# Optimization experiments

Hardware: AMD Instinct MI355X
Metric: run time of the kernel (lower is better)

The kernel has to match this reference:

```python
import jax, jax.numpy as jnp
import numpy as np

B, S_RAW, S_SUM, D_IN, H, NH = 32, 1024, 128, 300, 256, 4
DH = (2 * H) // NH  # per-head dim = 128


def _lstm_dir(x, Wih, Whh, b, reverse):
    """Single-direction LSTM (PyTorch gate order i,f,g,o). x: [B,S,D] -> [B,S,H]."""
    xg = jnp.einsum('bsd,gd->bsg', x, Wih) + b          # precompute input gates [B,S,4H]
    xg = jnp.swapaxes(xg, 0, 1)                          # [S,B,4H]
    Hh = Whh.shape[1]
    bsz = x.shape[0]

    def step(carry, g):
        h, c = carry
        gates = g + h @ Whh.T
        i, f, gg, o = jnp.split(gates, 4, axis=-1)
        c = jax.nn.sigmoid(f) * c + jax.nn.sigmoid(i) * jnp.tanh(gg)
        h = jax.nn.sigmoid(o) * jnp.tanh(c)
        return (h, c), h

    init = (jnp.zeros((bsz, Hh), x.dtype), jnp.zeros((bsz, Hh), x.dtype))
    _, hs = jax.lax.scan(step, init, xg, reverse=reverse)  # hs aligned with input time order
    return jnp.swapaxes(hs, 0, 1)


def _bilstm(x, pf, pb):
    return jnp.concatenate([_lstm_dir(x, *pf, False), _lstm_dir(x, *pb, True)], axis=-1)


def setup_inputs() -> dict:
    key = jax.random.key(0)
    ks = jax.random.split(key, 24)
    s_lstm = 1.0 / np.sqrt(H)
    s_proj = 1.0 / np.sqrt(2 * H)
    d = {}
    d['in_raw'] = jax.random.normal(ks[0], (B, S_RAW, D_IN), jnp.float32)
    d['in_sum'] = jax.random.normal(ks[1], (B, S_SUM, D_IN), jnp.float32)
    d['len_raw'] = jax.random.randint(ks[2], (B,), 0, S_RAW)
    d['len_sum'] = jax.random.randint(ks[3], (B,), 0, S_SUM)
    i = 4
    for name in ['raw_f', 'raw_b', 'sum_f', 'sum_b']:
        d[name + '_Wih'] = jax.random.uniform(ks[i], (4 * H, D_IN), jnp.float32, -s_lstm, s_lstm); i += 1
        d[name + '_Whh'] = jax.random.uniform(ks[i], (4 * H, H), jnp.float32, -s_lstm, s_lstm); i += 1
        d[name + '_b'] = jax.random.uniform(ks[i], (4 * H,), jnp.float32, -s_lstm, s_lstm); i += 1
    d['Wq'] = jax.random.uniform(ks[i], (NH, 2 * H, DH), jnp.float32, -s_proj, s_proj); i += 1
    d['Wk'] = jax.random.uniform(ks[i], (NH, 2 * H, DH), jnp.float32, -s_proj, s_proj); i += 1
    d['Wv'] = jax.random.uniform(ks[i], (NH, 2 * H, DH), jnp.float32, -s_proj, s_proj)
    return d


def reference(in_raw, in_sum, len_raw, len_sum,
              raw_f_Wih, raw_f_Whh, raw_f_b, raw_b_Wih, raw_b_Whh, raw_b_b,
              sum_f_Wih, sum_f_Whh, sum_f_b, sum_b_Wih, sum_b_Whh, sum_b_b,
              Wq, Wk, Wv):
    # BiLSTM encoders (dropout is identity in eval mode)
    out_raw = _bilstm(in_raw, (raw_f_Wih, raw_f_Whh, raw_f_b), (raw_b_Wih, raw_b_Whh, raw_b_b))  # [B,Sr,2H]
    out_sum = _bilstm(in_sum, (sum_f_Wih, sum_f_Whh, sum_f_b), (sum_b_Wih, sum_b_Whh, sum_b_b))  # [B,Ss,2H]

    # mean_pooling over the first len_sum[i] timesteps (lengths clamped to >=1)
    lens = jnp.maximum(len_sum, 1)
    mask = (jnp.arange(S_SUM)[None, :] < lens[:, None]).astype(out_sum.dtype)  # [B,Ss]
    sum_vec = jnp.einsum('bsd,bs->bd', out_sum, mask) / lens.astype(out_sum.dtype)[:, None]  # [B,2H]

    # per-head cross-attention against the single pooled summary vector (rank-1 attention)
    q = jnp.einsum('bsd,hde->hbse', out_raw, Wq)   # [NH,B,Sr,DH]
    k = jnp.einsum('bd,hde->hbe', sum_vec, Wk)     # [NH,B,DH]
    v = jnp.einsum('bd,hde->hbe', sum_vec, Wv)     # [NH,B,DH]
    scores = jnp.einsum('hbse,hbe->hbs', q, k)     # [NH,B,Sr] (use_divide_dk=False)
    attn = jax.nn.softmax(scores, axis=-1)
    rst = attn[..., None] * v[:, :, None, :] + q   # outer product + residual, [NH,B,Sr,DH]

    # concat heads along last dim -> [B,Sr,2H]
    rst = jnp.transpose(rst, (1, 2, 0, 3)).reshape(B, S_RAW, NH * DH)
    return rst
```

## Files before the change

### kernel.cpp

```cpp
#include <hip/hip_runtime.h>

typedef _Float16 f16;
typedef _Float16 half2t __attribute__((ext_vector_type(2)));
typedef _Float16 half8 __attribute__((ext_vector_type(8)));
typedef float f32x4 __attribute__((ext_vector_type(4)));

#define KP 320
#define DIN 300
#define SRAW 1024
#define SSUM 128

static constexpr size_t OFF_XG_RAW  = 0;
static constexpr size_t OFF_XG_SUM  = OFF_XG_RAW + (size_t)2*32*1024*1024*2;
static constexpr size_t OFF_OUT_RAW = OFF_XG_SUM + (size_t)2*32*128*1024*2;
static constexpr size_t OFF_OUT_SUM = OFF_OUT_RAW + (size_t)32*1024*512*2;
static constexpr size_t OFF_A_RAW   = OFF_OUT_SUM + (size_t)32*128*512*2;
static constexpr size_t OFF_A_SUM   = OFF_A_RAW + (size_t)32768*KP*2;
static constexpr size_t OFF_BIH_RAW = OFF_A_SUM + (size_t)4096*KP*2;
static constexpr size_t OFF_BIH_SUM = OFF_BIH_RAW + (size_t)2048*KP*2;
static constexpr size_t OFF_WHH     = OFF_BIH_SUM + (size_t)2048*KP*2;
static constexpr size_t OFF_WQ      = OFF_WHH + (size_t)4*32*1024*8*2;
static constexpr size_t OFF_KB      = OFF_WQ + (size_t)512*512*2;
static constexpr size_t OFF_VB      = OFF_KB + (size_t)4*32*128*4;
static constexpr size_t OFF_ATTN    = OFF_VB + (size_t)4*32*128*4;
static constexpr size_t WS_NEED     = OFF_ATTN + (size_t)4*32*1024*4;

__global__ void pack_kernel(
    const float* __restrict__ in_raw, const float* __restrict__ in_sum,
    const float* __restrict__ wih_rf, const float* __restrict__ wih_rb,
    const float* __restrict__ wih_sf, const float* __restrict__ wih_sb,
    const float* __restrict__ whh_rf, const float* __restrict__ whh_rb,
    const float* __restrict__ whh_sf, const float* __restrict__ whh_sb,
    const float* __restrict__ wq,
    f16* __restrict__ a_raw, f16* __restrict__ a_sum,
    f16* __restrict__ bih_raw, f16* __restrict__ bih_sum,
    f16* __restrict__ whh16, f16* __restrict__ wq16)
{
  constexpr size_t N1 = (size_t)32768*KP;
  constexpr size_t N2 = (size_t)4096*KP;
  constexpr size_t N3 = (size_t)2048*KP;
  constexpr size_t N5 = (size_t)4*32*1024*8;
  constexpr size_t N6 = (size_t)512*512;
  const size_t TOT = N1+N2+N3+N3+N5+N6;
  const size_t stride = (size_t)gridDim.x*blockDim.x;
  for (size_t i = (size_t)blockIdx.x*blockDim.x + threadIdx.x; i < TOT; i += stride) {
    size_t j = i;
    if (j < N1) {
      size_t m = j/KP, k = j - m*KP;
      a_raw[j] = (f16)(k < DIN ? in_raw[m*DIN + k] : 0.f);
      continue;
    }
    j -= N1;
    if (j < N2) {
      size_t m = j/KP, k = j - m*KP;
      a_sum[j] = (f16)(k < DIN ? in_sum[m*DIN + k] : 0.f);
      continue;
    }
    j -= N2;
    if (j < N3) {
      size_t n = j/KP, k = j - n*KP;
      float v = 0.f;
      if (k < DIN) v = (n < 1024) ? wih_rf[n*DIN + k] : wih_rb[(n-1024)*DIN + k];
      bih_raw[j] = (f16)v;
      continue;
    }
    j -= N3;
    if (j < N3) {
      size_t n = j/KP, k = j - n*KP;
      float v = 0.f;
      if (k < DIN) v = (n < 1024) ? wih_sf[n*DIN + k] : wih_sb[(n-1024)*DIN + k];
      bih_sum[j] = (f16)v;
      continue;
    }
    j -= N3;
    if (j < N5) {
      int ed  = (int)(j >> 18);
      int q   = (int)((j >> 13) & 31);
      int row = (int)((j >> 3) & 1023);
      int ii  = (int)(j & 7);
      const float* src = (ed==0)?whh_rf:(ed==1)?whh_rb:(ed==2)?whh_sf:whh_sb;
      whh16[j] = (f16)src[(size_t)row*256 + q*8 + ii];
      continue;
    }
    j -= N5;
    {
      int n = (int)(j >> 9), k = (int)(j & 511);
      int h = n >> 7, dh = n & 127;
      wq16[j] = (f16)wq[((size_t)h*512 + k)*128 + dh];
    }
  }
}

template<int EPI>
__global__ __launch_bounds__(256) void gemm_kernel(
    const f16* __restrict__ A, const f16* __restrict__ Bm,
    float* __restrict__ Cf, f16* __restrict__ Cx,
    const float* __restrict__ bias0, const float* __restrict__ bias1,
    int K, int ldcN, size_t dirStride)
{
  __shared__ __align__(16) f16 As[128*40];
  __shared__ __align__(16) f16 Bs[128*40];
  const int tid = threadIdx.x;
  const int m0 = blockIdx.x*128, n0 = blockIdx.y*128;
  const int w = tid >> 6, lane = tid & 63;
  const int wm = w >> 1, wn = w & 1;
  const int lr = lane & 15, lk = lane >> 4;
  f32x4 acc[4][4] = {};
  const int nsteps = K >> 5;
  for (int kt = 0; kt < nsteps; ++kt) {
    __syncthreads();
    #pragma unroll
    for (int it = 0; it < 2; ++it) {
      int c = tid + it*256;
      int r = c >> 2, kc = c & 3;
      *(uint4*)&As[r*40 + kc*8] = *(const uint4*)&A[(size_t)(m0+r)*K + kt*32 + kc*8];
      *(uint4*)&Bs[r*40 + kc*8] = *(const uint4*)&Bm[(size_t)(n0+r)*K + kt*32 + kc*8];
    }
    __syncthreads();
    half8 af[4], bf[4];
    #pragma unroll
    for (int mt = 0; mt < 4; ++mt) af[mt] = *(const half8*)&As[(wm*64 + mt*16 + lr)*40 + lk*8];
    #pragma unroll
    for (int nt = 0; nt < 4; ++nt) bf[nt] = *(const half8*)&Bs[(wn*64 + nt*16 + lr)*40 + lk*8];
    #pragma unroll
    for (int mt = 0; mt < 4; ++mt)
      #pragma unroll
      for (int nt = 0; nt < 4; ++nt)
        acc[mt][nt] = __builtin_amdgcn_mfma_f32_16x16x32_f16(af[mt], bf[nt], acc[mt][nt], 0, 0, 0);
  }
  const int rb = lk*4;
  #pragma unroll
  for (int mt = 0; mt < 4; ++mt) {
    #pragma unroll
    for (int nt = 0; nt < 4; ++nt) {
      int n = n0 + wn*64 + nt*16 + lr;
      int mloc = m0 + wm*64 + mt*16 + rb;
      if (EPI == 0) {
        #pragma unroll
        for (int r = 0; r < 4; ++r)
          Cf[(size_t)(mloc+r)*ldcN + n] = acc[mt][nt][r];
      } else {
        int dir = n >> 10, cc = n & 1023;
        float bs = (dir ? bias1 : bias0)[cc];
        f16* dst = Cx + (size_t)dir*dirStride;
        #pragma unroll
        for (int r = 0; r < 4; ++r)
          dst[(size_t)(mloc+r)*1024 + cc] = (f16)(acc[mt][nt][r] + bs);
      }
    }
  }
}

#define NREG 14
#define NLDS0 4
#define NLDS1 2
#define NGLB 12

__device__ __forceinline__ float dot8(float acc, uint4 wv, uint4 hv) {
#if __has_builtin(__builtin_amdgcn_fdot2)
  union { uint4 u; half2t h[4]; } W, Hh;
  W.u = wv; Hh.u = hv;
  #pragma unroll
  for (int i = 0; i < 4; ++i) acc = __builtin_amdgcn_fdot2(W.h[i], Hh.h[i], acc, false);
#else
  union { uint4 u; f16 h[8]; } W, Hh;
  W.u = wv; Hh.u = hv;
  #pragma unroll
  for (int i = 0; i < 8; ++i) acc += (float)W.h[i]*(float)Hh.h[i];
#endif
  return acc;
}

__global__ __launch_bounds__(1024) void lstm_kernel(
    const f16* __restrict__ whh16,
    const f16* __restrict__ xg_raw, const f16* __restrict__ xg_sum,
    f16* __restrict__ out_raw, f16* __restrict__ out_sum)
{
  const int wg = blockIdx.x;
  const int e = wg >> 6, r2 = wg & 63, d = r2 >> 5, b = r2 & 31;
  const int S = e ? SSUM : SRAW;
  const int t = threadIdx.x;
  const f16* wbase = whh16 + (size_t)(e*2+d)*(32*1024*8);
  const uint4* wreg_g = (const uint4*)wbase;
  const uint4* wl0_g  = (const uint4*)(wbase + (size_t)NREG*1024*8);
  const uint4* wl1_g  = (const uint4*)(wbase + (size_t)(NREG+NLDS0)*1024*8);
  const uint4* wglb_g = (const uint4*)(wbase + (size_t)(NREG+NLDS0+NLDS1)*1024*8);
  const f16* xg = (e ? xg_sum : xg_raw) + ((size_t)(d*32 + b))*(size_t)S*1024;
  f16* outp = (e ? out_sum : out_raw) + (size_t)b*S*512 + d*256;

  __shared__ __align__(16) f16 wl0[NLDS0*1024*8];
  __shared__ __align__(16) f16 wl1[NLDS1*1024*8];
  __shared__ __align__(16) f16 hl[256];
  __shared__ float pre[1024];

  uint4 wr[NREG];
  #pragma unroll
  for (int j = 0; j < NREG; ++j) wr[j] = wreg_g[j*1024 + t];
  #pragma unroll
  for (int j = 0; j < NLDS0; ++j) *(uint4*)&wl0[(j*1024 + t)*8] = wl0_g[j*1024 + t];
  #pragma unroll
  for (int j = 0; j < NLDS1; ++j) *(uint4*)&wl1[(j*1024 + t)*8] = wl1_g[j*1024 + t];
  if (t < 256) hl[t] = (f16)0.f;
  float cst = 0.f;
  __syncthreads();

  for (int st = 0; st < S; ++st) {
    const int s = d ? (S - 1 - st) : st;
    float xv = (float)xg[(size_t)s*1024 + t];
    float acc = 0.f;
    uint4 g0 = wglb_g[t],          g1 = wglb_g[1024 + t],  g2 = wglb_g[2*1024 + t],
          g3 = wglb_g[3*1024 + t], g4 = wglb_g[4*1024 + t], g5 = wglb_g[5*1024 + t];
    #pragma unroll
    for (int q = 0; q < NREG; ++q) {
      uint4 hv = *(const uint4*)&hl[q*8];
      acc = dot8(acc, wr[q], hv);
    }
    #pragma unroll
    for (int j = 0; j < NLDS0; ++j) {
      uint4 hv = *(const uint4*)&hl[(NREG + j)*8];
      uint4 wv = *(const uint4*)&wl0[(j*1024 + t)*8];
      acc = dot8(acc, wv, hv);
    }
    #pragma unroll
    for (int j = 0; j < NLDS1; ++j) {
      uint4 hv = *(const uint4*)&hl[(NREG + NLDS0 + j)*8];
      uint4 wv = *(const uint4*)&wl1[(j*1024 + t)*8];
      acc = dot8(acc, wv, hv);
    }
    uint4 g6 = wglb_g[6*1024 + t], g7 = wglb_g[7*1024 + t], g8 = wglb_g[8*1024 + t],
          g9 = wglb_g[9*1024 + t], g10 = wglb_g[10*1024 + t], g11 = wglb_g[11*1024 + t];
    { uint4 hv = *(const uint4*)&hl[20*8]; acc = dot8(acc, g0, hv); }
    { uint4 hv = *(const uint4*)&hl[21*8]; acc = dot8(acc, g1, hv); }
    { uint4 hv = *(const uint4*)&hl[22*8]; acc = dot8(acc, g2, hv); }
    { uint4 hv = *(const uint4*)&hl[23*8]; acc = dot8(acc, g3, hv); }
    { uint4 hv = *(const uint4*)&hl[24*8]; acc = dot8(acc, g4, hv); }
    { uint4 hv = *(const uint4*)&hl[25*8]; acc = dot8(acc, g5, hv); }
    { uint4 hv = *(const uint4*)&hl[26*8]; acc = dot8(acc, g6, hv); }
    { uint4 hv = *(const uint4*)&hl[27*8]; acc = dot8(acc, g7, hv); }
    { uint4 hv = *(const uint4*)&hl[28*8]; acc = dot8(acc, g8, hv); }
    { uint4 hv = *(const uint4*)&hl[29*8]; acc = dot8(acc, g9, hv); }
    { uint4 hv = *(const uint4*)&hl[30*8]; acc = dot8(acc, g10, hv); }
    { uint4 hv = *(const uint4*)&hl[31*8]; acc = dot8(acc, g11, hv); }
    acc += xv;
    pre[t] = acc;
    __syncthreads();
    if (t < 256) {
      float pi = pre[t], pf = pre[t+256], pg = pre[t+512], po = pre[t+768];
      float ig = 1.f/(1.f + __expf(-pi));
      float fg = 1.f/(1.f + __expf(-pf));
      float gg = tanhf(pg);
      float og = 1.f/(1.f + __expf(-po));
      cst = fg*cst + ig*gg;
      float hval = og*tanhf(cst);
      f16 hf = (f16)hval;
      hl[t] = hf;
      outp[(size_t)s*512 + t] = hf;
    }
    __syncthreads();
  }
}

__global__ __launch_bounds__(256) void pool_kv_kernel(
    const f16* __restrict__ out_sum, const int* __restrict__ len_sum,
    const float* __restrict__ Wk, const float* __restrict__ Wv,
    float* __restrict__ kb, float* __restrict__ vb)
{
  const int b = blockIdx.x, t = threadIdx.x;
  __shared__ float sv[512];
  int len = len_sum[b]; if (len < 1) len = 1;
  float a0 = 0.f, a1 = 0.f;
  for (int s = 0; s < len; ++s) {
    const f16* row = out_sum + ((size_t)b*SSUM + s)*512;
    a0 += (float)row[t];
    a1 += (float)row[t+256];
  }
  float inv = 1.f/(float)len;
  sv[t] = a0*inv; sv[t+256] = a1*inv;
  __syncthreads();
  #pragma unroll
  for (int half = 0; half < 2; ++half) {
    int o = t + half*256;
    int h = o >> 7, dh = o & 127;
    const float* wkp = Wk + (size_t)h*512*128 + dh;
    const float* wvp = Wv + (size_t)h*512*128 + dh;
    float ak = 0.f, av = 0.f;
    for (int e2 = 0; e2 < 512; ++e2) {
      float sve = sv[e2];
      ak += sve*wkp[(size_t)e2*128];
      av += sve*wvp[(size_t)e2*128];
    }
    kb[((size_t)h*32 + b)*128 + dh] = ak;
    vb[((size_t)h*32 + b)*128 + dh] = av;
  }
}

__global__ __launch_bounds__(256) void attn_kernel(
    const float* __restrict__ q, const float* __restrict__ kb, float* __restrict__ attn)
{
  const int hb = blockIdx.x;
  const int h = hb >> 5, b = hb & 31;
  const int t = threadIdx.x;
  __shared__ __align__(16) float kk[128];
  __shared__ float red[4];
  if (t < 128) kk[t] = kb[(size_t)hb*128 + t];
  __syncthreads();
  float vals[4];
  #pragma unroll
  for (int i = 0; i < 4; ++i) {
    int s = t + i*256;
    const float4* qp = (const float4*)(q + ((size_t)b*1024 + s)*512 + h*128);
    const float4* kp = (const float4*)kk;
    float a = 0.f;
    #pragma unroll
    for (int e2 = 0; e2 < 32; ++e2) {
      float4 qq = qp[e2], kx = kp[e2];
      a += qq.x*kx.x + qq.y*kx.y + qq.z*kx.z + qq.w*kx.w;
    }
    vals[i] = a;
  }
  float m = fmaxf(fmaxf(vals[0], vals[1]), fmaxf(vals[2], vals[3]));
  for (int o = 1; o < 64; o <<= 1) m = fmaxf(m, __shfl_xor(m, o));
  if ((t & 63) == 0) red[t >> 6] = m;
  __syncthreads();
  m = fmaxf(fmaxf(red[0], red[1]), fmaxf(red[2], red[3]));
  __syncthreads();
  float ex[4], lsum = 0.f;
  #pragma unroll
  for (int i = 0; i < 4; ++i) { ex[i] = __expf(vals[i] - m); lsum += ex[i]; }
  for (int o = 1; o < 64; o <<= 1) lsum += __shfl_xor(lsum, o);
  if ((t & 63) == 0) red[t >> 6] = lsum;
  __syncthreads();
  float inv = 1.f/(red[0] + red[1] + red[2] + red[3]);
  #pragma unroll
  for (int i = 0; i < 4; ++i) attn[(size_t)hb*1024 + t + i*256] = ex[i]*inv;
}

__global__ __launch_bounds__(256) void final_kernel(
    float* __restrict__ out, const float* __restrict__ attn, const float* __restrict__ vb)
{
  const size_t TOT4 = (size_t)32*1024*512/4;
  const size_t stride = (size_t)gridDim.x*blockDim.x;
  for (size_t i = (size_t)blockIdx.x*blockDim.x + threadIdx.x; i < TOT4; i += stride) {
    int c4 = (int)(i & 127);
    int h = c4 >> 5;
    size_t srow = i >> 7;
    int b = (int)(srow >> 10), s = (int)(srow & 1023);
    float a = attn[((size_t)h*32 + b)*1024 + s];
    float4 vv = ((const float4*)vb)[((size_t)h*32 + b)*32 + (c4 & 31)];
    float4 qq = ((float4*)out)[i];
    qq.x += a*vv.x; qq.y += a*vv.y; qq.z += a*vv.z; qq.w += a*vv.w;
    ((float4*)out)[i] = qq;
  }
}

extern "C" void kernel_launch(void* const* d_in, const int* in_sizes, int n_in,
                              void* d_out, int out_size, void* d_ws, size_t ws_size,
                              hipStream_t stream)
{
  const float* in_raw = (const float*)d_in[0];
  const float* in_sum = (const float*)d_in[1];
  const int*  len_sum = (const int*)d_in[3];
  const float* rf_wih = (const float*)d_in[4];
  const float* rf_whh = (const float*)d_in[5];
  const float* rf_b   = (const float*)d_in[6];
  const float* rb_wih = (const float*)d_in[7];
  const float* rb_whh = (const float*)d_in[8];
  const float* rb_b   = (const float*)d_in[9];
  const float* sf_wih = (const float*)d_in[10];
  const float* sf_whh = (const float*)d_in[11];
  const float* sf_b   = (const float*)d_in[12];
  const float* sb_wih = (const float*)d_in[13];
  const float* sb_whh = (const float*)d_in[14];
  const float* sb_b   = (const float*)d_in[15];
  const float* wq     = (const float*)d_in[16];
  const float* wk     = (const float*)d_in[17];
  const float* wv     = (const float*)d_in[18];

  if (ws_size < WS_NEED) return;

  char* ws = (char*)d_ws;
  f16* xg_raw_p  = (f16*)(ws + OFF_XG_RAW);
  f16* xg_sum_p  = (f16*)(ws + OFF_XG_SUM);
  f16* out_raw_p = (f16*)(ws + OFF_OUT_RAW);
  f16* out_sum_p = (f16*)(ws + OFF_OUT_SUM);
  f16* a_raw_p   = (f16*)(ws + OFF_A_RAW);
  f16* a_sum_p   = (f16*)(ws + OFF_A_SUM);
  f16* bih_raw_p = (f16*)(ws + OFF_BIH_RAW);
  f16* bih_sum_p = (f16*)(ws + OFF_BIH_SUM);
  f16* whh16_p   = (f16*)(ws + OFF_WHH);
  f16* wq16_p    = (f16*)(ws + OFF_WQ);
  float* kb_p    = (float*)(ws + OFF_KB);
  float* vb_p    = (float*)(ws + OFF_VB);
  float* attn_p  = (float*)(ws + OFF_ATTN);
  float* qout    = (float*)d_out;

  pack_kernel<<<4096, 256, 0, stream>>>(
      in_raw, in_sum, rf_wih, rb_wih, sf_wih, sb_wih,
      rf_whh, rb_whh, sf_whh, sb_whh, wq,
      a_raw_p, a_sum_p, bih_raw_p, bih_sum_p, whh16_p, wq16_p);

  gemm_kernel<1><<<dim3(256, 16), 256, 0, stream>>>(
      a_raw_p, bih_raw_p, nullptr, xg_raw_p, rf_b, rb_b, KP, 0, (size_t)32*1024*1024);
  gemm_kernel<1><<<dim3(32, 16), 256, 0, stream>>>(
      a_sum_p, bih_sum_p, nullptr, xg_sum_p, sf_b, sb_b, KP, 0, (size_t)32*128*1024);

  lstm_kernel<<<128, 1024, 0, stream>>>(whh16_p, xg_raw_p, xg_sum_p, out_raw_p, out_sum_p);

  gemm_kernel<0><<<dim3(256, 4), 256, 0, stream>>>(
      out_raw_p, wq16_p, qout, nullptr, nullptr, nullptr, 512, 512, 0);

  pool_kv_kernel<<<32, 256, 0, stream>>>(out_sum_p, len_sum, wk, wv, kb_p, vb_p);
  attn_kernel<<<128, 256, 0, stream>>>(qout, kb_p, attn_p);
  final_kernel<<<4096, 256, 0, stream>>>(qout, attn_p, vb_p);
}
```

Before: 2.476 ms.

## Halve LSTM block to 512 threads, two gate rows per thread, distributed activations

The recurrent LSTM kernel now runs 512 threads per block, with each thread computing two gate rows. Weights are rebalanced: more stay in registers (24 chunks per row), 5 chunks go to LDS, and only 3 are streamed from global memory each step. Gate activations are applied by the threads that compute them, using fast rcp-based sigmoid/tanh, and only the f/o values pass through LDS. The input-gate value for the next step is prefetched one step ahead. The aim is shorter per-step latency from fewer global loads and less serial activation work, at the cost of much higher register pressure and reduced activation accuracy.

After: 2.132 ms. 1.16x faster.

```diff
diff --git a/kernel.cpp b/kernel.cpp
--- a/kernel.cpp
+++ b/kernel.cpp
@@ -151,10 +151,9 @@
   }
 }
 
-#define NREG 14
-#define NLDS0 4
-#define NLDS1 2
-#define NGLB 12
+#define NREG 24
+#define NLDS 5
+#define NGLB 3
 
 __device__ __forceinline__ float dot8(float acc, uint4 wv, uint4 hv) {
 #if __has_builtin(__builtin_amdgcn_fdot2)
@@ -171,7 +170,16 @@
   return acc;
 }
 
-__global__ __launch_bounds__(1024) void lstm_kernel(
+__device__ __forceinline__ float sigmoid_f(float x) {
+  float e = __expf(-x);
+  return __builtin_amdgcn_rcpf(1.f + e);
+}
+__device__ __forceinline__ float tanh_f(float x) {
+  float e = __expf(2.f * x);
+  return 1.f - 2.f * __builtin_amdgcn_rcpf(e + 1.f);
+}
+
+__global__ __launch_bounds__(512, 2) void lstm_kernel(
     const f16* __restrict__ whh16,
     const f16* __restrict__ xg_raw, const f16* __restrict__ xg_sum,
     f16* __restrict__ out_raw, f16* __restrict__ out_sum)
@@ -182,76 +190,73 @@
   const int t = threadIdx.x;
   const f16* wbase = whh16 + (size_t)(e*2+d)*(32*1024*8);
   const uint4* wreg_g = (const uint4*)wbase;
-  const uint4* wl0_g  = (const uint4*)(wbase + (size_t)NREG*1024*8);
-  const uint4* wl1_g  = (const uint4*)(wbase + (size_t)(NREG+NLDS0)*1024*8);
-  const uint4* wglb_g = (const uint4*)(wbase + (size_t)(NREG+NLDS0+NLDS1)*1024*8);
+  const uint4* wlds_g = (const uint4*)(wbase + (size_t)NREG*1024*8);
+  const uint4* wglb_g = (const uint4*)(wbase + (size_t)(NREG+NLDS)*1024*8);
   const f16* xg = (e ? xg_sum : xg_raw) + ((size_t)(d*32 + b))*(size_t)S*1024;
   f16* outp = (e ? out_sum : out_raw) + (size_t)b*S*512 + d*256;
 
-  __shared__ __align__(16) f16 wl0[NLDS0*1024*8];
-  __shared__ __align__(16) f16 wl1[NLDS1*1024*8];
+  __shared__ __align__(16) f16 wl[NLDS*1024*8];
   __shared__ __align__(16) f16 hl[256];
-  __shared__ float pre[1024];
-
-  uint4 wr[NREG];
-  #pragma unroll
-  for (int j = 0; j < NREG; ++j) wr[j] = wreg_g[j*1024 + t];
-  #pragma unroll
-  for (int j = 0; j < NLDS0; ++j) *(uint4*)&wl0[(j*1024 + t)*8] = wl0_g[j*1024 + t];
-  #pragma unroll
-  for (int j = 0; j < NLDS1; ++j) *(uint4*)&wl1[(j*1024 + t)*8] = wl1_g[j*1024 + t];
+  __shared__ float exf[256];
+  __shared__ float exo[256];
+
+  uint4 wrA[NREG], wrB[NREG];
+  #pragma unroll
+  for (int j = 0; j < NREG; ++j) {
+    wrA[j] = wreg_g[j*1024 + t];
+    wrB[j] = wreg_g[j*1024 + t + 512];
+  }
+  for (int i = t; i < NLDS*1024; i += 512) ((uint4*)wl)[i] = wlds_g[i];
   if (t < 256) hl[t] = (f16)0.f;
   float cst = 0.f;
+  const int s0 = d ? (S - 1) : 0;
+  f16 xcA = xg[(size_t)s0*1024 + t];
+  f16 xcB = xg[(size_t)s0*1024 + t + 512];
   __syncthreads();
 
   for (int st = 0; st < S; ++st) {
     const int s = d ? (S - 1 - st) : st;
-    float xv = (float)xg[(size_t)s*1024 + t];
-    float acc = 0.f;
-    uint4 g0 = wglb_g[t],          g1 = wglb_g[1024 + t],  g2 = wglb_g[2*1024 + t],
-          g3 = wglb_g[3*1024 + t], g4 = wglb_g[4*1024 + t], g5 = wglb_g[5*1024 + t];
+    uint4 gA0 = wglb_g[t],        gB0 = wglb_g[t + 512];
+    uint4 gA1 = wglb_g[1024 + t], gB1 = wglb_g[1024 + t + 512];
+    uint4 gA2 = wglb_g[2048 + t], gB2 = wglb_g[2048 + t + 512];
+    f16 xnA = (f16)0.f, xnB = (f16)0.f;
+    if (st + 1 < S) {
+      const int sn = d ? (S - 2 - st) : (st + 1);
+      xnA = xg[(size_t)sn*1024 + t];
+      xnB = xg[(size_t)sn*1024 + t + 512];
+    }
+    float accA = (float)xcA, accB = (float)xcB;
     #pragma unroll
     for (int q = 0; q < NREG; ++q) {
       uint4 hv = *(const uint4*)&hl[q*8];
-      acc = dot8(acc, wr[q], hv);
-    }
-    #pragma unroll
-    for (int j = 0; j < NLDS0; ++j) {
+      accA = dot8(accA, wrA[q], hv);
+      accB = dot8(accB, wrB[q], hv);
+    }
+    #pragma unroll
+    for (int j = 0; j < NLDS; ++j) {
       uint4 hv = *(const uint4*)&hl[(NREG + j)*8];
-      uint4 wv = *(const uint4*)&wl0[(j*1024 + t)*8];
-      acc = dot8(acc, wv, hv);
-    }
-    #pragma unroll
-    for (int j = 0; j < NLDS1; ++j) {
-      uint4 hv = *(const uint4*)&hl[(NREG + NLDS0 + j)*8];
-      uint4 wv = *(const uint4*)&wl1[(j*1024 + t)*8];
-      acc = dot8(acc, wv, hv);
-    }
-    uint4 g6 = wglb_g[6*1024 + t], g7 = wglb_g[7*1024 + t], g8 = wglb_g[8*1024 + t],
-          g9 = wglb_g[9*1024 + t], g10 = wglb_g[10*1024 + t], g11 = wglb_g[11*1024 + t];
-    { uint4 hv = *(const uint4*)&hl[20*8]; acc = dot8(acc, g0, hv); }
-    { uint4 hv = *(const uint4*)&hl[21*8]; acc = dot8(acc, g1, hv); }
-    { uint4 hv = *(const uint4*)&hl[22*8]; acc = dot8(acc, g2, hv); }
-    { uint4 hv = *(const uint4*)&hl[23*8]; acc = dot8(acc, g3, hv); }
-    { uint4 hv = *(const uint4*)&hl[24*8]; acc = dot8(acc, g4, hv); }
-    { uint4 hv = *(const uint4*)&hl[25*8]; acc = dot8(acc, g5, hv); }
-    { uint4 hv = *(const uint4*)&hl[26*8]; acc = dot8(acc, g6, hv); }
-    { uint4 hv = *(const uint4*)&hl[27*8]; acc = dot8(acc, g7, hv); }
-    { uint4 hv = *(const uint4*)&hl[28*8]; acc = dot8(acc, g8, hv); }
-    { uint4 hv = *(const uint4*)&hl[29*8]; acc = dot8(acc, g9, hv); }
-    { uint4 hv = *(const uint4*)&hl[30*8]; acc = dot8(acc, g10, hv); }
-    { uint4 hv = *(const uint4*)&hl[31*8]; acc = dot8(acc, g11, hv); }
-    acc += xv;
-    pre[t] = acc;
+      uint4 wvA = *(const uint4*)&wl[((size_t)(j*1024 + t))*8];
+      uint4 wvB = *(const uint4*)&wl[((size_t)(j*1024 + t + 512))*8];
+      accA = dot8(accA, wvA, hv);
+      accB = dot8(accB, wvB, hv);
+    }
+    { uint4 hv = *(const uint4*)&hl[(NREG+NLDS+0)*8]; accA = dot8(accA, gA0, hv); accB = dot8(accB, gB0, hv); }
+    { uint4 hv = *(const uint4*)&hl[(NREG+NLDS+1)*8]; accA = dot8(accA, gA1, hv); accB = dot8(accB, gB1, hv); }
+    { uint4 hv = *(const uint4*)&hl[(NREG+NLDS+2)*8]; accA = dot8(accA, gA2, hv); accB = dot8(accB, gB2, hv); }
+    float aA = sigmoid_f(accA);
+    float aB;
+    if (t < 256) {
+      aB = tanh_f(accB);
+    } else {
+      aB = sigmoid_f(accB);
+      exf[t - 256] = aA;
+      exo[t - 256] = aB;
+    }
+    xcA = xnA; xcB = xnB;
     __syncthreads();
     if (t < 256) {
-      float pi = pre[t], pf = pre[t+256], pg = pre[t+512], po = pre[t+768];
-      float ig = 1.f/(1.f + __expf(-pi));
-      float fg = 1.f/(1.f + __expf(-pf));
-      float gg = tanhf(pg);
-      float og = 1.f/(1.f + __expf(-po));
-      cst = fg*cst + ig*gg;
-      float hval = og*tanhf(cst);
+      cst = exf[t]*cst + aA*aB;
+      float hval = exo[t]*tanh_f(cst);
       f16 hf = (f16)hval;
       hl[t] = hf;
       outp[(size_t)s*512 + t] = hf;
@@ -404,7 +409,7 @@
   gemm_kernel<1><<<dim3(32, 16), 256, 0, stream>>>(
       a_sum_p, bih_sum_p, nullptr, xg_sum_p, sf_b, sb_b, KP, 0, (size_t)32*128*1024);
 
-  lstm_kernel<<<128, 1024, 0, stream>>>(whh16_p, xg_raw_p, xg_sum_p, out_raw_p, out_sum_p);
+  lstm_kernel<<<128, 512, 0, stream>>>(whh16_p, xg_raw_p, xg_sum_p, out_raw_p, out_sum_p);
 
   gemm_kernel<0><<<dim3(256, 4), 256, 0, stream>>>(
       out_raw_p, wq16_p, qout, nullptr, nullptr, nullptr, 512, 512, 0);
```
